# Kernel tuning notes

Hardware: AMD Instinct MI355X
Metric: run time of the kernel (lower is better)

Reference implementation:

```python
import jax, jax.numpy as jnp
import numpy as np

B, C, H, W = 2, 512, 64, 64
NH = 8
EPS = 1e-5


def setup_inputs() -> dict:
    key = jax.random.key(0)
    ks = jax.random.split(key, 4)
    s_in = 1.0 / np.sqrt(C)
    x = jax.random.normal(ks[0], (B, C, H, W), dtype=jnp.float32)
    qkv_w = jax.random.normal(ks[1], (3 * C, C), dtype=jnp.float32) * s_in
    qkv_b = jnp.zeros((3 * C,), dtype=jnp.float32)
    out_w = jax.random.normal(ks[2], (C, C), dtype=jnp.float32) * s_in
    out_b = jnp.zeros((C,), dtype=jnp.float32)
    ln_g = jnp.ones((C,), dtype=jnp.float32)
    ln_b = jnp.zeros((C,), dtype=jnp.float32)
    return {"x": x, "qkv_w": qkv_w, "qkv_b": qkv_b, "out_w": out_w,
            "out_b": out_b, "ln_g": ln_g, "ln_b": ln_b, "num_heads": NH}


def reference(x, qkv_w, qkv_b, out_w, out_b, ln_g, ln_b, num_heads):
    b, c, h, w = x.shape
    n = h * w
    hd = c // num_heads
    scale = hd ** -0.5

    # flatten spatial: [B, N, C]
    tokens = x.reshape(b, c, n).transpose(0, 2, 1)

    # fused QKV projection
    qkv = tokens @ qkv_w.T + qkv_b            # [B, N, 3C]
    q, k, v = jnp.split(qkv, 3, axis=-1)

    def heads(t):  # [B, N, C] -> [B, H, N, D]
        return t.reshape(b, n, num_heads, hd).transpose(0, 2, 1, 3)

    q, k, v = heads(q), heads(k), heads(v)

    # naive full attention (materializes [B, H, N, N] as in the original)
    scores = jnp.einsum('bhqd,bhkd->bhqk', q, k) * scale
    attn = jax.nn.softmax(scores, axis=-1)
    out = jnp.einsum('bhqk,bhkd->bhqd', attn, v)  # [B, H, N, D]

    out = out.transpose(0, 2, 1, 3).reshape(b, n, c)
    attended = out @ out_w.T + out_b          # [B, N, C]

    # residual + LayerNorm over channels
    res = attended + tokens
    mean = jnp.mean(res, axis=-1, keepdims=True)
    var = jnp.var(res, axis=-1, keepdims=True)
    y = (res - mean) * jax.lax.rsqrt(var + EPS) * ln_g + ln_b

    return y.transpose(0, 2, 1).reshape(b, c, h, w)
```

## Files before the change

### kernel.cpp

```cpp
#include <hip/hip_runtime.h>

#define BATCH 2
#define CH    512
#define NTOK  4096
#define NH    8
#define HD    64
#define MTOT  (BATCH*NTOK)

typedef __attribute__((ext_vector_type(8))) __bf16 bf16x8;
typedef __attribute__((ext_vector_type(4))) float  f32x4;
typedef __attribute__((ext_vector_type(4))) unsigned short u16x4;

static __device__ __forceinline__ f32x4 mfma16(bf16x8 a, bf16x8 b, f32x4 c) {
  return __builtin_amdgcn_mfma_f32_16x16x32_bf16(a, b, c, 0, 0, 0);
}

static __device__ __forceinline__ unsigned short f2bf(float f) {
  unsigned int u = __float_as_uint(f);
  u += 0x7fffu + ((u >> 16) & 1u);
  return (unsigned short)(u >> 16);
}

static __device__ __forceinline__ void gload_lds16(const unsigned short* g, unsigned short* l) {
  __builtin_amdgcn_global_load_lds((const __attribute__((address_space(1))) void*)g,
                                   (__attribute__((address_space(3))) void*)l, 16, 0, 0);
}

#define QSC 0.18033688011112042f

__global__ __launch_bounds__(256) void k_transpose(const float* __restrict__ x,
                                                   unsigned short* __restrict__ tokB) {
  __shared__ float tile[32][33];
  int b  = blockIdx.z;
  int n0 = blockIdx.x * 32;
  int c0 = blockIdx.y * 32;
  int tx = threadIdx.x & 31, ty = threadIdx.x >> 5;
#pragma unroll
  for (int i = 0; i < 4; i++) {
    int c = c0 + ty + 8 * i;
    tile[ty + 8 * i][tx] = x[((size_t)b * CH + c) * NTOK + n0 + tx];
  }
  __syncthreads();
#pragma unroll
  for (int i = 0; i < 4; i++) {
    int n = n0 + ty + 8 * i;
    int c = c0 + tx;
    tokB[((size_t)b * NTOK + n) * CH + c] = f2bf(tile[tx][ty + 8 * i]);
  }
}

__global__ __launch_bounds__(256) void k_castw(const float* __restrict__ w1,
                                               const float* __restrict__ w2,
                                               unsigned short* __restrict__ o1,
                                               unsigned short* __restrict__ o2) {
  int i = blockIdx.x * 256 + threadIdx.x;
  if (i < 3 * CH * CH) o1[i] = f2bf(w1[i]);
  else o2[i - 3 * CH * CH] = f2bf(w2[i - 3 * CH * CH]);
}

#define BK 64

static __device__ __forceinline__ void stage_g(const unsigned short* __restrict__ src,
                                               size_t row0, int k0,
                                               unsigned short* __restrict__ lds,
                                               int wid, int lane) {
  int sub = lane >> 3;
  int ch  = (lane & 7) ^ sub;
#pragma unroll
  for (int i = 0; i < 4; i++) {
    int rbase = 32 * wid + 8 * i;
    gload_lds16(&src[(row0 + rbase + sub) * 512 + k0 + ch * 8], &lds[rbase * BK]);
  }
}

static __device__ __forceinline__ void stage_g64(const unsigned short* __restrict__ src,
                                                 size_t row0, int k0,
                                                 unsigned short* __restrict__ lds,
                                                 int wid, int lane) {
  int sub = lane >> 3;
  int ch  = (lane & 7) ^ sub;
#pragma unroll
  for (int i = 0; i < 2; i++) {
    int rbase = 16 * wid + 8 * i;
    gload_lds16(&src[(row0 + rbase + sub) * 512 + k0 + ch * 8], &lds[rbase * BK]);
  }
}

static __device__ __forceinline__ bf16x8 frag_ld(const unsigned short* __restrict__ lds,
                                                 int row, int ks, int lane) {
  int ch = ((ks << 2) + (lane >> 4)) ^ (row & 7);
  return *reinterpret_cast<const bf16x8*>(&lds[row * BK + ch * 8]);
}

__global__ __launch_bounds__(256) void k_gemm_qkv(const unsigned short* __restrict__ A,
                                                  const unsigned short* __restrict__ W,
                                                  const float* __restrict__ bias,
                                                  unsigned short* __restrict__ qb,
                                                  unsigned short* __restrict__ kb,
                                                  unsigned short* __restrict__ vt) {
  __shared__ unsigned short lsA[128 * BK];
  __shared__ unsigned short lsB[128 * BK];
  int bm0 = blockIdx.x * 128;
  int bn0 = blockIdx.y * 128;
  int tid = threadIdx.x, lane = tid & 63, wid = tid >> 6;
  int wm = wid >> 1, wn = wid & 1;

  f32x4 acc[4][4];
  f32x4 zz = {0.f, 0.f, 0.f, 0.f};
#pragma unroll
  for (int i = 0; i < 4; i++)
#pragma unroll
    for (int j = 0; j < 4; j++) acc[i][j] = zz;

  for (int k0 = 0; k0 < 512; k0 += BK) {
    stage_g(A, (size_t)bm0, k0, lsA, wid, lane);
    stage_g(W, (size_t)bn0, k0, lsB, wid, lane);
    __syncthreads();
#pragma unroll
    for (int ks = 0; ks < 2; ks++) {
      bf16x8 af[4], bfr[4];
#pragma unroll
      for (int t = 0; t < 4; t++) {
        af[t]  = frag_ld(lsA, wm * 64 + t * 16 + (lane & 15), ks, lane);
        bfr[t] = frag_ld(lsB, wn * 64 + t * 16 + (lane & 15), ks, lane);
      }
#pragma unroll
      for (int mt = 0; mt < 4; mt++)
#pragma unroll
        for (int nt = 0; nt < 4; nt++) acc[mt][nt] = mfma16(af[mt], bfr[nt], acc[mt][nt]);
    }
    __syncthreads();
  }
#pragma unroll
  for (int nt = 0; nt < 4; nt++) {
    int j = bn0 + wn * 64 + nt * 16 + (lane & 15);
    float bj = bias[j];
    int which = j >> 9;
    int cp = j & 511;
    int h = cp >> 6, d = cp & 63;
    if (which == 2) {
#pragma unroll
      for (int mt = 0; mt < 4; mt++) {
        int m = bm0 + wm * 64 + mt * 16 + 4 * (lane >> 4);
        int b = m >> 12, n = m & 4095;
        u16x4 pk;
#pragma unroll
        for (int r = 0; r < 4; r++) pk[r] = f2bf(acc[mt][nt][r] + bj);
        *reinterpret_cast<u16x4*>(&vt[((size_t)((b * NH + h) * HD + d)) * NTOK + n]) = pk;
      }
    } else {
      unsigned short* dst = (which == 0) ? qb : kb;
      float sc = (which == 0) ? QSC : 1.0f;
#pragma unroll
      for (int mt = 0; mt < 4; mt++) {
#pragma unroll
        for (int r = 0; r < 4; r++) {
          int m = bm0 + wm * 64 + mt * 16 + 4 * (lane >> 4) + r;
          int b = m >> 12, n = m & 4095;
          dst[(((size_t)(b * NH + h) * NTOK + n) << 6) + d] = f2bf((acc[mt][nt][r] + bj) * sc);
        }
      }
    }
  }
}

#define KVB 128
#define NT  (NTOK / KVB)

static __device__ __forceinline__ void stage_kv(const unsigned short* __restrict__ Kp,
                                                const unsigned short* __restrict__ Vp,
                                                unsigned short* __restrict__ lk,
                                                unsigned short* __restrict__ lv,
                                                int kv0, int wid, int lane) {
  int sub = lane >> 3;
  int c7  = lane & 7;
  int sub4 = lane >> 4;
  int c15  = lane & 15;
#pragma unroll
  for (int i = 0; i < 4; i++) {
    int rbase = 32 * wid + 8 * i;
    int fk = (sub & 3) | ((i & 1) << 2);
    gload_lds16(&Kp[((size_t)(kv0 + rbase + sub) << 6) + ((c7 ^ fk) << 3)], &lk[rbase << 6]);
    int rbv = 16 * wid + 4 * i;
    int fv = 4 * i + sub4;
    gload_lds16(&Vp[(size_t)(rbv + sub4) * NTOK + kv0 + ((c15 ^ fv) << 3)], &lv[rbv << 7]);
  }
}

static __device__ __forceinline__ void attn_tile(const unsigned short* __restrict__ lk,
                                                 const unsigned short* __restrict__ lv,
                                                 int h,
                                                 const bf16x8 qf[2][2],
                                                 f32x4* oacc0, f32x4* oacc1,
                                                 f32x4& lacc0, f32x4& lacc1,
                                                 bf16x8 onesf, int g, int lr) {
  f32x4 zz = {0.f, 0.f, 0.f, 0.f};
  int l7 = lr & 7;
  int tbase = 8 * (lr >> 2) + (lr & 3);
  int kc0 = ((g ^ l7) << 3);
  int kc1 = (((4 + g) ^ l7) << 3);
  bf16x8 kf[4][2];
#pragma unroll
  for (int ct = 0; ct < 4; ct++) {
    int t = tbase + 4 * (ct >> 1) + 32 * (ct & 1);
    kf[ct][0] = *reinterpret_cast<const bf16x8*>(&lk[(t << 6) + kc0]);
    kf[ct][1] = *reinterpret_cast<const bf16x8*>(&lk[(t << 6) + kc1]);
  }
  f32x4 s0[4], s1[4];
#pragma unroll
  for (int ct = 0; ct < 4; ct++) {
    s0[ct] = zz; s1[ct] = zz;
#pragma unroll
    for (int ks = 0; ks < 2; ks++) {
      s0[ct] = mfma16(kf[ct][ks], qf[0][ks], s0[ct]);
      s1[ct] = mfma16(kf[ct][ks], qf[1][ks], s1[ct]);
    }
  }
  bf16x8 vf[4][2];
#pragma unroll
  for (int dt = 0; dt < 4; dt++) {
    int rowb = (dt * 16 + lr) << 7;
    vf[dt][0] = *reinterpret_cast<const bf16x8*>(&lv[rowb + ((((h << 3) + g) ^ lr) << 3)]);
    vf[dt][1] = *reinterpret_cast<const bf16x8*>(&lv[rowb + ((((h << 3) + 4 + g) ^ lr) << 3)]);
  }
#pragma unroll
  for (int ct = 0; ct < 4; ct++) {
#pragma unroll
    for (int r = 0; r < 4; r++) {
      s0[ct][r] = __builtin_exp2f(s0[ct][r]);
      s1[ct][r] = __builtin_exp2f(s1[ct][r]);
    }
  }
  unsigned int w0[4][2], w1[4][2];
#pragma unroll
  for (int ct = 0; ct < 4; ct++) {
    asm("v_cvt_pk_bf16_f32 %0, %1, %2" : "=v"(w0[ct][0]) : "v"(s0[ct][0]), "v"(s0[ct][1]));
    asm("v_cvt_pk_bf16_f32 %0, %1, %2" : "=v"(w0[ct][1]) : "v"(s0[ct][2]), "v"(s0[ct][3]));
    asm("v_cvt_pk_bf16_f32 %0, %1, %2" : "=v"(w1[ct][0]) : "v"(s1[ct][0]), "v"(s1[ct][1]));
    asm("v_cvt_pk_bf16_f32 %0, %1, %2" : "=v"(w1[ct][1]) : "v"(s1[ct][2]), "v"(s1[ct][3]));
  }
  union U { unsigned int w[4]; bf16x8 v; };
  U a0, a1, b0, b1;
  a0.w[0] = w0[0][0]; a0.w[1] = w0[0][1]; a0.w[2] = w0[2][0]; a0.w[3] = w0[2][1];
  a1.w[0] = w0[1][0]; a1.w[1] = w0[1][1]; a1.w[2] = w0[3][0]; a1.w[3] = w0[3][1];
  b0.w[0] = w1[0][0]; b0.w[1] = w1[0][1]; b0.w[2] = w1[2][0]; b0.w[3] = w1[2][1];
  b1.w[0] = w1[1][0]; b1.w[1] = w1[1][1]; b1.w[2] = w1[3][0]; b1.w[3] = w1[3][1];
#pragma unroll
  for (int dt = 0; dt < 4; dt++) {
    oacc0[dt] = mfma16(a0.v, vf[dt][0], oacc0[dt]);
    oacc0[dt] = mfma16(a1.v, vf[dt][1], oacc0[dt]);
    oacc1[dt] = mfma16(b0.v, vf[dt][0], oacc1[dt]);
    oacc1[dt] = mfma16(b1.v, vf[dt][1], oacc1[dt]);
  }
  lacc0 = mfma16(a0.v, onesf, lacc0);
  lacc0 = mfma16(a1.v, onesf, lacc0);
  lacc1 = mfma16(b0.v, onesf, lacc1);
  lacc1 = mfma16(b1.v, onesf, lacc1);
}

__global__ __launch_bounds__(256, 2) void k_attn(const unsigned short* __restrict__ Q,
                                                 const unsigned short* __restrict__ K,
                                                 const unsigned short* __restrict__ Vt,
                                                 unsigned short* __restrict__ O) {
  __shared__ unsigned short lsK[2][KVB * 64];
  __shared__ unsigned short lsV[2][64 * KVB];
  int gid = blockIdx.y * 32 + blockIdx.x;
  int vv  = (gid & 7) * 64 + (gid >> 3);
  int bh  = vv >> 5;
  int tid = threadIdx.x, lane = tid & 63, wid = tid >> 6;
  int g = lane >> 4, lr = lane & 15;
  int qw = (vv & 31) * 128 + wid * 32;
  const unsigned short* Qp = Q + (size_t)bh * NTOK * HD;
  const unsigned short* Kp = K + (size_t)bh * NTOK * HD;
  const unsigned short* Vp = Vt + (size_t)bh * HD * NTOK;
  unsigned short* K0 = &lsK[0][0]; unsigned short* K1 = &lsK[1][0];
  unsigned short* V0 = &lsV[0][0]; unsigned short* V1 = &lsV[1][0];

  union { unsigned short u[8]; bf16x8 v; } ou;
#pragma unroll
  for (int i = 0; i < 8; i++) ou.u[i] = 0x3F80;
  bf16x8 onesf = ou.v;

  bf16x8 qf[2][2];
#pragma unroll
  for (int sq = 0; sq < 2; sq++)
#pragma unroll
    for (int ks = 0; ks < 2; ks++)
      qf[sq][ks] = *reinterpret_cast<const bf16x8*>(
          &Qp[(size_t)(qw + sq * 16 + lr) * HD + ks * 32 + 8 * g]);

  f32x4 zz = {0.f, 0.f, 0.f, 0.f};
  f32x4 oacc0[4] = {zz, zz, zz, zz};
  f32x4 oacc1[4] = {zz, zz, zz, zz};
  f32x4 lacc0 = zz, lacc1 = zz;

  stage_kv(Kp, Vp, K0, V0, 0, wid, lane);
  __syncthreads();

  for (int t = 0; t < NT; t += 2) {
    stage_kv(Kp, Vp, K1, V1, (t + 1) * KVB, wid, lane);
    attn_tile(K0,        V0, 0, qf, oacc0, oacc1, lacc0, lacc1, onesf, g, lr);
    attn_tile(K0 + 4096, V0, 1, qf, oacc0, oacc1, lacc0, lacc1, onesf, g, lr);
    __syncthreads();
    if (t + 2 < NT) stage_kv(Kp, Vp, K0, V0, (t + 2) * KVB, wid, lane);
    attn_tile(K1,        V1, 0, qf, oacc0, oacc1, lacc0, lacc1, onesf, g, lr);
    attn_tile(K1 + 4096, V1, 1, qf, oacc0, oacc1, lacc0, lacc1, onesf, g, lr);
    __syncthreads();
  }
  int b2 = bh >> 3, h = bh & 7;
#pragma unroll
  for (int sq = 0; sq < 2; sq++) {
    f32x4* oacc = sq ? oacc1 : oacc0;
    f32x4  lacc = sq ? lacc1 : lacc0;
#pragma unroll
    for (int r = 0; r < 4; r++) {
      float inv = 1.0f / lacc[r];
      int n = qw + sq * 16 + 4 * g + r;
#pragma unroll
      for (int dt = 0; dt < 4; dt++) {
        int d = dt * 16 + lr;
        O[((size_t)(b2 * NTOK + n)) * CH + h * HD + d] = f2bf(oacc[dt][r] * inv);
      }
    }
  }
}

__global__ __launch_bounds__(256) void k_gemm_out(const unsigned short* __restrict__ A,
                                                  const unsigned short* __restrict__ W,
                                                  const float* __restrict__ bias,
                                                  const unsigned short* __restrict__ tokB,
                                                  unsigned short* __restrict__ res) {
  __shared__ unsigned short lsA[64 * BK];
  __shared__ unsigned short lsB[128 * BK];
  int bm0 = blockIdx.x * 64;
  int bn0 = blockIdx.y * 128;
  int tid = threadIdx.x, lane = tid & 63, wid = tid >> 6;
  int wm = wid >> 1, wn = wid & 1;

  f32x4 acc[2][4];
  f32x4 zz = {0.f, 0.f, 0.f, 0.f};
#pragma unroll
  for (int i = 0; i < 2; i++)
#pragma unroll
    for (int j = 0; j < 4; j++) acc[i][j] = zz;

  for (int k0 = 0; k0 < 512; k0 += BK) {
    stage_g64(A, (size_t)bm0, k0, lsA, wid, lane);
    stage_g(W, (size_t)bn0, k0, lsB, wid, lane);
    __syncthreads();
#pragma unroll
    for (int ks = 0; ks < 2; ks++) {
      bf16x8 af[2], bfr[4];
#pragma unroll
      for (int t = 0; t < 2; t++)
        af[t] = frag_ld(lsA, wm * 32 + t * 16 + (lane & 15), ks, lane);
#pragma unroll
      for (int t = 0; t < 4; t++)
        bfr[t] = frag_ld(lsB, wn * 64 + t * 16 + (lane & 15), ks, lane);
#pragma unroll
      for (int mt = 0; mt < 2; mt++)
#pragma unroll
        for (int nt = 0; nt < 4; nt++) acc[mt][nt] = mfma16(af[mt], bfr[nt], acc[mt][nt]);
    }
    __syncthreads();
  }
#pragma unroll
  for (int nt = 0; nt < 4; nt++) {
    int j = bn0 + wn * 64 + nt * 16 + (lane & 15);
    float bj = bias[j];
#pragma unroll
    for (int mt = 0; mt < 2; mt++) {
#pragma unroll
      for (int r = 0; r < 4; r++) {
        int m = bm0 + wm * 32 + mt * 16 + 4 * (lane >> 4) + r;
        size_t idx = (size_t)m * CH + j;
        float tk = __uint_as_float((unsigned int)tokB[idx] << 16);
        res[idx] = f2bf(acc[mt][nt][r] + bj + tk);
      }
    }
  }
}

__global__ __launch_bounds__(256) void k_ln(const unsigned short* __restrict__ res,
                                            const float* __restrict__ g,
                                            const float* __restrict__ bb,
                                            float* __restrict__ y) {
  __shared__ float smean[64], srstd[64];
  int m0 = blockIdx.x * 64;
  int tid = threadIdx.x, lane = tid & 63, wid = tid >> 6;
  for (int t = 0; t < 16; t++) {
    int idx = wid * 16 + t;
    uint4 v = *reinterpret_cast<const uint4*>(&res[(size_t)(m0 + idx) * CH + lane * 8]);
    unsigned int wv[4] = {v.x, v.y, v.z, v.w};
    float s = 0.f, ss = 0.f;
#pragma unroll
    for (int j = 0; j < 4; j++) {
      float lo = __uint_as_float(wv[j] << 16);
      float hi = __uint_as_float(wv[j] & 0xFFFF0000u);
      s += lo + hi; ss += lo * lo + hi * hi;
    }
#pragma unroll
    for (int off = 1; off < 64; off <<= 1) {
      s += __shfl_xor(s, off);
      ss += __shfl_xor(ss, off);
    }
    if (lane == 0) {
      float mean = s * (1.0f / CH);
      float var = ss * (1.0f / CH) - mean * mean;
      smean[idx] = mean;
      srstd[idx] = rsqrtf(var + 1e-5f);
    }
  }
  __syncthreads();
  int b = m0 >> 12, n0 = m0 & 4095;
  int tn = tid & 63;
  int cq = tid >> 6;
  float mn = smean[tn], rs = srstd[tn];
  const unsigned short* rrow = res + (size_t)(m0 + tn) * CH;
  float* yb = y + ((size_t)b * CH) * NTOK + n0 + tn;
#pragma unroll
  for (int i = 0; i < 16; i++) {
    int c = cq * 128 + i * 8;
    uint4 v = *reinterpret_cast<const uint4*>(&rrow[c]);
    unsigned int wv[4] = {v.x, v.y, v.z, v.w};
    float4 ga = *reinterpret_cast<const float4*>(&g[c]);
    float4 gb = *reinterpret_cast<const float4*>(&g[c + 4]);
    float4 ba = *reinterpret_cast<const float4*>(&bb[c]);
    float4 b4 = *reinterpret_cast<const float4*>(&bb[c + 4]);
    float gg[8] = {ga.x, ga.y, ga.z, ga.w, gb.x, gb.y, gb.z, gb.w};
    float bv[8] = {ba.x, ba.y, ba.z, ba.w, b4.x, b4.y, b4.z, b4.w};
#pragma unroll
    for (int j = 0; j < 4; j++) {
      float lo = __uint_as_float(wv[j] << 16);
      float hi = __uint_as_float(wv[j] & 0xFFFF0000u);
      yb[(size_t)(c + 2 * j) * NTOK]     = (lo - mn) * rs * gg[2 * j]     + bv[2 * j];
      yb[(size_t)(c + 2 * j + 1) * NTOK] = (hi - mn) * rs * gg[2 * j + 1] + bv[2 * j + 1];
    }
  }
}

extern "C" void kernel_launch(void* const* d_in, const int* in_sizes, int n_in,
                              void* d_out, int out_size, void* d_ws, size_t ws_size,
                              hipStream_t stream) {
  const float* x    = (const float*)d_in[0];
  const float* qkvw = (const float*)d_in[1];
  const float* qkvb = (const float*)d_in[2];
  const float* outw = (const float*)d_in[3];
  const float* outb = (const float*)d_in[4];
  const float* lng  = (const float*)d_in[5];
  const float* lnb  = (const float*)d_in[6];
  float* y = (float*)d_out;

  const size_t NC = (size_t)MTOT * CH;
  char* ws = (char*)d_ws;
  size_t off = 0;
  auto nxt = [&](size_t bytes) -> void* {
    void* p = ws + off;
    off += (bytes + 255) & ~(size_t)255;
    return p;
  };
  unsigned short* tokB = (unsigned short*)nxt(NC * 2);
  unsigned short* wqkv = (unsigned short*)nxt((size_t)3 * CH * CH * 2);
  unsigned short* wout = (unsigned short*)nxt((size_t)CH * CH * 2);
  unsigned short* qb   = (unsigned short*)nxt(NC * 2);
  unsigned short* kb   = (unsigned short*)nxt(NC * 2);
  unsigned short* vt   = (unsigned short*)nxt(NC * 2);
  unsigned short* ao   = (unsigned short*)nxt(NC * 2);
  unsigned short* resb = (unsigned short*)nxt(NC * 2);
  if (off > ws_size) return;

  k_transpose<<<dim3(NTOK / 32, CH / 32, BATCH), 256, 0, stream>>>(x, tokB);
  k_castw<<<(4 * CH * CH) / 256, 256, 0, stream>>>(qkvw, outw, wqkv, wout);
  k_gemm_qkv<<<dim3(MTOT / 128, (3 * CH) / 128), 256, 0, stream>>>(tokB, wqkv, qkvb, qb, kb, vt);
  k_attn<<<dim3(32, 16), 256, 0, stream>>>(qb, kb, vt, ao);
  k_gemm_out<<<dim3(MTOT / 64, CH / 128), 256, 0, stream>>>(ao, wout, outb, tokB, resb);
  k_ln<<<MTOT / 64, 256, 0, stream>>>(resb, lng, lnb, y);
}
```

Baseline: 164.0 us.

## Shrink attention tiles to 16 queries per wave and 64-key KV blocks

Restructures the attention kernel so each wave handles 16 query rows instead of 32, and each block stages 64 keys per step instead of 128. The V LDS layout and swizzle are simplified to match. The grid doubles to 1024 blocks, and launch bounds now target 4 blocks per CU, to raise occupancy and reduce register pressure. In exchange, K/V reuse per loaded tile is halved, so LDS reads and global traffic grow relative to MFMA work.

```diff
diff --git a/kernel.cpp b/kernel.cpp
--- a/kernel.cpp
+++ b/kernel.cpp
@@ -164,7 +164,7 @@
   }
 }
 
-#define KVB 128
+#define KVB 64
 #define NT  (NTOK / KVB)
 
 static __device__ __forceinline__ void stage_kv(const unsigned short* __restrict__ Kp,
@@ -174,25 +174,20 @@
                                                 int kv0, int wid, int lane) {
   int sub = lane >> 3;
   int c7  = lane & 7;
-  int sub4 = lane >> 4;
-  int c15  = lane & 15;
-#pragma unroll
-  for (int i = 0; i < 4; i++) {
-    int rbase = 32 * wid + 8 * i;
-    int fk = (sub & 3) | ((i & 1) << 2);
-    gload_lds16(&Kp[((size_t)(kv0 + rbase + sub) << 6) + ((c7 ^ fk) << 3)], &lk[rbase << 6]);
-    int rbv = 16 * wid + 4 * i;
-    int fv = 4 * i + sub4;
-    gload_lds16(&Vp[(size_t)(rbv + sub4) * NTOK + kv0 + ((c15 ^ fv) << 3)], &lv[rbv << 7]);
+#pragma unroll
+  for (int i = 0; i < 2; i++) {
+    int rbase = 16 * wid + 8 * i;
+    int row = rbase + sub;
+    int fk = (sub & 3) | (i << 2);
+    gload_lds16(&Kp[((size_t)(kv0 + row) << 6) + ((c7 ^ fk) << 3)], &lk[rbase << 6]);
+    gload_lds16(&Vp[(size_t)row * NTOK + kv0 + ((c7 ^ sub) << 3)], &lv[rbase << 6]);
   }
 }
 
 static __device__ __forceinline__ void attn_tile(const unsigned short* __restrict__ lk,
                                                  const unsigned short* __restrict__ lv,
-                                                 int h,
-                                                 const bf16x8 qf[2][2],
-                                                 f32x4* oacc0, f32x4* oacc1,
-                                                 f32x4& lacc0, f32x4& lacc1,
+                                                 const bf16x8 qf[2],
+                                                 f32x4* oacc, f32x4& lacc,
                                                  bf16x8 onesf, int g, int lr) {
   f32x4 zz = {0.f, 0.f, 0.f, 0.f};
   int l7 = lr & 7;
@@ -206,70 +201,55 @@
     kf[ct][0] = *reinterpret_cast<const bf16x8*>(&lk[(t << 6) + kc0]);
     kf[ct][1] = *reinterpret_cast<const bf16x8*>(&lk[(t << 6) + kc1]);
   }
-  f32x4 s0[4], s1[4];
+  f32x4 s[4];
 #pragma unroll
   for (int ct = 0; ct < 4; ct++) {
-    s0[ct] = zz; s1[ct] = zz;
-#pragma unroll
-    for (int ks = 0; ks < 2; ks++) {
-      s0[ct] = mfma16(kf[ct][ks], qf[0][ks], s0[ct]);
-      s1[ct] = mfma16(kf[ct][ks], qf[1][ks], s1[ct]);
-    }
+    s[ct] = mfma16(kf[ct][0], qf[0], zz);
+    s[ct] = mfma16(kf[ct][1], qf[1], s[ct]);
   }
   bf16x8 vf[4][2];
 #pragma unroll
   for (int dt = 0; dt < 4; dt++) {
-    int rowb = (dt * 16 + lr) << 7;
-    vf[dt][0] = *reinterpret_cast<const bf16x8*>(&lv[rowb + ((((h << 3) + g) ^ lr) << 3)]);
-    vf[dt][1] = *reinterpret_cast<const bf16x8*>(&lv[rowb + ((((h << 3) + 4 + g) ^ lr) << 3)]);
+    int rowb = (dt * 16 + lr) << 6;
+    vf[dt][0] = *reinterpret_cast<const bf16x8*>(&lv[rowb + kc0]);
+    vf[dt][1] = *reinterpret_cast<const bf16x8*>(&lv[rowb + kc1]);
   }
 #pragma unroll
   for (int ct = 0; ct < 4; ct++) {
 #pragma unroll
-    for (int r = 0; r < 4; r++) {
-      s0[ct][r] = __builtin_exp2f(s0[ct][r]);
-      s1[ct][r] = __builtin_exp2f(s1[ct][r]);
-    }
-  }
-  unsigned int w0[4][2], w1[4][2];
+    for (int r = 0; r < 4; r++) s[ct][r] = __builtin_exp2f(s[ct][r]);
+  }
+  unsigned int w[4][2];
 #pragma unroll
   for (int ct = 0; ct < 4; ct++) {
-    asm("v_cvt_pk_bf16_f32 %0, %1, %2" : "=v"(w0[ct][0]) : "v"(s0[ct][0]), "v"(s0[ct][1]));
-    asm("v_cvt_pk_bf16_f32 %0, %1, %2" : "=v"(w0[ct][1]) : "v"(s0[ct][2]), "v"(s0[ct][3]));
-    asm("v_cvt_pk_bf16_f32 %0, %1, %2" : "=v"(w1[ct][0]) : "v"(s1[ct][0]), "v"(s1[ct][1]));
-    asm("v_cvt_pk_bf16_f32 %0, %1, %2" : "=v"(w1[ct][1]) : "v"(s1[ct][2]), "v"(s1[ct][3]));
+    asm("v_cvt_pk_bf16_f32 %0, %1, %2" : "=v"(w[ct][0]) : "v"(s[ct][0]), "v"(s[ct][1]));
+    asm("v_cvt_pk_bf16_f32 %0, %1, %2" : "=v"(w[ct][1]) : "v"(s[ct][2]), "v"(s[ct][3]));
   }
   union U { unsigned int w[4]; bf16x8 v; };
-  U a0, a1, b0, b1;
-  a0.w[0] = w0[0][0]; a0.w[1] = w0[0][1]; a0.w[2] = w0[2][0]; a0.w[3] = w0[2][1];
-  a1.w[0] = w0[1][0]; a1.w[1] = w0[1][1]; a1.w[2] = w0[3][0]; a1.w[3] = w0[3][1];
-  b0.w[0] = w1[0][0]; b0.w[1] = w1[0][1]; b0.w[2] = w1[2][0]; b0.w[3] = w1[2][1];
-  b1.w[0] = w1[1][0]; b1.w[1] = w1[1][1]; b1.w[2] = w1[3][0]; b1.w[3] = w1[3][1];
+  U a0, a1;
+  a0.w[0] = w[0][0]; a0.w[1] = w[0][1]; a0.w[2] = w[2][0]; a0.w[3] = w[2][1];
+  a1.w[0] = w[1][0]; a1.w[1] = w[1][1]; a1.w[2] = w[3][0]; a1.w[3] = w[3][1];
 #pragma unroll
   for (int dt = 0; dt < 4; dt++) {
-    oacc0[dt] = mfma16(a0.v, vf[dt][0], oacc0[dt]);
-    oacc0[dt] = mfma16(a1.v, vf[dt][1], oacc0[dt]);
-    oacc1[dt] = mfma16(b0.v, vf[dt][0], oacc1[dt]);
-    oacc1[dt] = mfma16(b1.v, vf[dt][1], oacc1[dt]);
-  }
-  lacc0 = mfma16(a0.v, onesf, lacc0);
-  lacc0 = mfma16(a1.v, onesf, lacc0);
-  lacc1 = mfma16(b0.v, onesf, lacc1);
-  lacc1 = mfma16(b1.v, onesf, lacc1);
-}
-
-__global__ __launch_bounds__(256, 2) void k_attn(const unsigned short* __restrict__ Q,
+    oacc[dt] = mfma16(a0.v, vf[dt][0], oacc[dt]);
+    oacc[dt] = mfma16(a1.v, vf[dt][1], oacc[dt]);
+  }
+  lacc = mfma16(a0.v, onesf, lacc);
+  lacc = mfma16(a1.v, onesf, lacc);
+}
+
+__global__ __launch_bounds__(256, 4) void k_attn(const unsigned short* __restrict__ Q,
                                                  const unsigned short* __restrict__ K,
                                                  const unsigned short* __restrict__ Vt,
                                                  unsigned short* __restrict__ O) {
   __shared__ unsigned short lsK[2][KVB * 64];
   __shared__ unsigned short lsV[2][64 * KVB];
-  int gid = blockIdx.y * 32 + blockIdx.x;
-  int vv  = (gid & 7) * 64 + (gid >> 3);
-  int bh  = vv >> 5;
+  int gid = blockIdx.x;
+  int vv  = (gid & 7) * 128 + (gid >> 3);
+  int bh  = vv >> 6;
   int tid = threadIdx.x, lane = tid & 63, wid = tid >> 6;
   int g = lane >> 4, lr = lane & 15;
-  int qw = (vv & 31) * 128 + wid * 32;
+  int qw = (vv & 63) * 64 + wid * 16;
   const unsigned short* Qp = Q + (size_t)bh * NTOK * HD;
   const unsigned short* Kp = K + (size_t)bh * NTOK * HD;
   const unsigned short* Vp = Vt + (size_t)bh * HD * NTOK;
@@ -281,46 +261,36 @@
   for (int i = 0; i < 8; i++) ou.u[i] = 0x3F80;
   bf16x8 onesf = ou.v;
 
-  bf16x8 qf[2][2];
-#pragma unroll
-  for (int sq = 0; sq < 2; sq++)
-#pragma unroll
-    for (int ks = 0; ks < 2; ks++)
-      qf[sq][ks] = *reinterpret_cast<const bf16x8*>(
-          &Qp[(size_t)(qw + sq * 16 + lr) * HD + ks * 32 + 8 * g]);
+  bf16x8 qf[2];
+#pragma unroll
+  for (int ks = 0; ks < 2; ks++)
+    qf[ks] = *reinterpret_cast<const bf16x8*>(
+        &Qp[(size_t)(qw + lr) * HD + ks * 32 + 8 * g]);
 
   f32x4 zz = {0.f, 0.f, 0.f, 0.f};
-  f32x4 oacc0[4] = {zz, zz, zz, zz};
-  f32x4 oacc1[4] = {zz, zz, zz, zz};
-  f32x4 lacc0 = zz, lacc1 = zz;
+  f32x4 oacc[4] = {zz, zz, zz, zz};
+  f32x4 lacc = zz;
 
   stage_kv(Kp, Vp, K0, V0, 0, wid, lane);
   __syncthreads();
 
   for (int t = 0; t < NT; t += 2) {
     stage_kv(Kp, Vp, K1, V1, (t + 1) * KVB, wid, lane);
-    attn_tile(K0,        V0, 0, qf, oacc0, oacc1, lacc0, lacc1, onesf, g, lr);
-    attn_tile(K0 + 4096, V0, 1, qf, oacc0, oacc1, lacc0, lacc1, onesf, g, lr);
+    attn_tile(K0, V0, qf, oacc, lacc, onesf, g, lr);
     __syncthreads();
     if (t + 2 < NT) stage_kv(Kp, Vp, K0, V0, (t + 2) * KVB, wid, lane);
-    attn_tile(K1,        V1, 0, qf, oacc0, oacc1, lacc0, lacc1, onesf, g, lr);
-    attn_tile(K1 + 4096, V1, 1, qf, oacc0, oacc1, lacc0, lacc1, onesf, g, lr);
+    attn_tile(K1, V1, qf, oacc, lacc, onesf, g, lr);
     __syncthreads();
   }
   int b2 = bh >> 3, h = bh & 7;
 #pragma unroll
-  for (int sq = 0; sq < 2; sq++) {
-    f32x4* oacc = sq ? oacc1 : oacc0;
-    f32x4  lacc = sq ? lacc1 : lacc0;
-#pragma unroll
-    for (int r = 0; r < 4; r++) {
-      float inv = 1.0f / lacc[r];
-      int n = qw + sq * 16 + 4 * g + r;
-#pragma unroll
-      for (int dt = 0; dt < 4; dt++) {
-        int d = dt * 16 + lr;
-        O[((size_t)(b2 * NTOK + n)) * CH + h * HD + d] = f2bf(oacc[dt][r] * inv);
-      }
+  for (int r = 0; r < 4; r++) {
+    float inv = 1.0f / lacc[r];
+    int n = qw + 4 * g + r;
+#pragma unroll
+    for (int dt = 0; dt < 4; dt++) {
+      int d = dt * 16 + lr;
+      O[((size_t)(b2 * NTOK + n)) * CH + h * HD + d] = f2bf(oacc[dt][r] * inv);
     }
   }
 }
@@ -472,7 +442,7 @@
   k_transpose<<<dim3(NTOK / 32, CH / 32, BATCH), 256, 0, stream>>>(x, tokB);
   k_castw<<<(4 * CH * CH) / 256, 256, 0, stream>>>(qkvw, outw, wqkv, wout);
   k_gemm_qkv<<<dim3(MTOT / 128, (3 * CH) / 128), 256, 0, stream>>>(tokB, wqkv, qkvb, qb, kb, vt);
-  k_attn<<<dim3(32, 16), 256, 0, stream>>>(qb, kb, vt, ao);
+  k_attn<<<1024, 256, 0, stream>>>(qb, kb, vt, ao);
   k_gemm_out<<<dim3(MTOT / 64, CH / 128), 256, 0, stream>>>(ao, wout, outb, tokB, resb);
   k_ln<<<MTOT / 64, 256, 0, stream>>>(resb, lng, lnb, y);
 }
```

New measurement: 169.5 us. +3.3%, slower.

## Split KV tiles across wave pairs in attention and merge partial sums via LDS

Applied to the files above, without the earlier changes.

The attention kernel now gives each block 64 queries instead of 128 and launches 1024 blocks. Within a block, pairs of waves split each 64-key tile in half, and the two halves' partial output and denominator sums are combined through LDS at the end. The KV tile shrinks to 64, which cuts LDS use and permits four blocks per CU, aiming for more parallelism and occupancy. In exchange, each K/V tile is reused by fewer queries, so global traffic and the number of syncs per key rise, and there is an extra reduction step.

```diff
diff --git a/kernel.cpp b/kernel.cpp
--- a/kernel.cpp
+++ b/kernel.cpp
@@ -164,7 +164,7 @@
   }
 }
 
-#define KVB 128
+#define KVB 64
 #define NT  (NTOK / KVB)
 
 static __device__ __forceinline__ void stage_kv(const unsigned short* __restrict__ Kp,
@@ -174,102 +174,90 @@
                                                 int kv0, int wid, int lane) {
   int sub = lane >> 3;
   int c7  = lane & 7;
-  int sub4 = lane >> 4;
-  int c15  = lane & 15;
-#pragma unroll
-  for (int i = 0; i < 4; i++) {
-    int rbase = 32 * wid + 8 * i;
-    int fk = (sub & 3) | ((i & 1) << 2);
-    gload_lds16(&Kp[((size_t)(kv0 + rbase + sub) << 6) + ((c7 ^ fk) << 3)], &lk[rbase << 6]);
-    int rbv = 16 * wid + 4 * i;
-    int fv = 4 * i + sub4;
-    gload_lds16(&Vp[(size_t)(rbv + sub4) * NTOK + kv0 + ((c15 ^ fv) << 3)], &lv[rbv << 7]);
+#pragma unroll
+  for (int i = 0; i < 2; i++) {
+    int rbase = 16 * wid + 8 * i;
+    int row = rbase + sub;
+    int fk = (sub & 3) | (i << 2);
+    gload_lds16(&Kp[((size_t)(kv0 + row) << 6) + ((c7 ^ fk) << 3)], &lk[rbase << 6]);
+    gload_lds16(&Vp[(size_t)row * NTOK + kv0 + ((c7 ^ sub) << 3)], &lv[rbase << 6]);
   }
 }
 
 static __device__ __forceinline__ void attn_tile(const unsigned short* __restrict__ lk,
                                                  const unsigned short* __restrict__ lv,
-                                                 int h,
+                                                 int half,
                                                  const bf16x8 qf[2][2],
                                                  f32x4* oacc0, f32x4* oacc1,
                                                  f32x4& lacc0, f32x4& lacc1,
                                                  bf16x8 onesf, int g, int lr) {
   f32x4 zz = {0.f, 0.f, 0.f, 0.f};
   int l7 = lr & 7;
-  int tbase = 8 * (lr >> 2) + (lr & 3);
-  int kc0 = ((g ^ l7) << 3);
-  int kc1 = (((4 + g) ^ l7) << 3);
-  bf16x8 kf[4][2];
-#pragma unroll
-  for (int ct = 0; ct < 4; ct++) {
-    int t = tbase + 4 * (ct >> 1) + 32 * (ct & 1);
+  int tbase = 32 * half + 8 * (lr >> 2) + (lr & 3);
+  int kc0 = (g ^ l7) << 3;
+  int kc1 = ((4 + g) ^ l7) << 3;
+  bf16x8 kf[2][2];
+#pragma unroll
+  for (int ct = 0; ct < 2; ct++) {
+    int t = tbase + 4 * ct;
     kf[ct][0] = *reinterpret_cast<const bf16x8*>(&lk[(t << 6) + kc0]);
     kf[ct][1] = *reinterpret_cast<const bf16x8*>(&lk[(t << 6) + kc1]);
   }
-  f32x4 s0[4], s1[4];
-#pragma unroll
-  for (int ct = 0; ct < 4; ct++) {
-    s0[ct] = zz; s1[ct] = zz;
-#pragma unroll
-    for (int ks = 0; ks < 2; ks++) {
-      s0[ct] = mfma16(kf[ct][ks], qf[0][ks], s0[ct]);
-      s1[ct] = mfma16(kf[ct][ks], qf[1][ks], s1[ct]);
-    }
-  }
-  bf16x8 vf[4][2];
-#pragma unroll
-  for (int dt = 0; dt < 4; dt++) {
-    int rowb = (dt * 16 + lr) << 7;
-    vf[dt][0] = *reinterpret_cast<const bf16x8*>(&lv[rowb + ((((h << 3) + g) ^ lr) << 3)]);
-    vf[dt][1] = *reinterpret_cast<const bf16x8*>(&lv[rowb + ((((h << 3) + 4 + g) ^ lr) << 3)]);
-  }
-#pragma unroll
-  for (int ct = 0; ct < 4; ct++) {
+  f32x4 s0[2], s1[2];
+#pragma unroll
+  for (int ct = 0; ct < 2; ct++) {
+    s0[ct] = mfma16(kf[ct][0], qf[0][0], zz);
+    s0[ct] = mfma16(kf[ct][1], qf[0][1], s0[ct]);
+    s1[ct] = mfma16(kf[ct][0], qf[1][0], zz);
+    s1[ct] = mfma16(kf[ct][1], qf[1][1], s1[ct]);
+  }
+  bf16x8 vf[4];
+  int vc = (((half << 2) + g) ^ l7) << 3;
+#pragma unroll
+  for (int dt = 0; dt < 4; dt++)
+    vf[dt] = *reinterpret_cast<const bf16x8*>(&lv[((dt * 16 + lr) << 6) + vc]);
+#pragma unroll
+  for (int ct = 0; ct < 2; ct++) {
 #pragma unroll
     for (int r = 0; r < 4; r++) {
       s0[ct][r] = __builtin_exp2f(s0[ct][r]);
       s1[ct][r] = __builtin_exp2f(s1[ct][r]);
     }
   }
-  unsigned int w0[4][2], w1[4][2];
-#pragma unroll
-  for (int ct = 0; ct < 4; ct++) {
+  unsigned int w0[2][2], w1[2][2];
+#pragma unroll
+  for (int ct = 0; ct < 2; ct++) {
     asm("v_cvt_pk_bf16_f32 %0, %1, %2" : "=v"(w0[ct][0]) : "v"(s0[ct][0]), "v"(s0[ct][1]));
     asm("v_cvt_pk_bf16_f32 %0, %1, %2" : "=v"(w0[ct][1]) : "v"(s0[ct][2]), "v"(s0[ct][3]));
     asm("v_cvt_pk_bf16_f32 %0, %1, %2" : "=v"(w1[ct][0]) : "v"(s1[ct][0]), "v"(s1[ct][1]));
     asm("v_cvt_pk_bf16_f32 %0, %1, %2" : "=v"(w1[ct][1]) : "v"(s1[ct][2]), "v"(s1[ct][3]));
   }
   union U { unsigned int w[4]; bf16x8 v; };
-  U a0, a1, b0, b1;
-  a0.w[0] = w0[0][0]; a0.w[1] = w0[0][1]; a0.w[2] = w0[2][0]; a0.w[3] = w0[2][1];
-  a1.w[0] = w0[1][0]; a1.w[1] = w0[1][1]; a1.w[2] = w0[3][0]; a1.w[3] = w0[3][1];
-  b0.w[0] = w1[0][0]; b0.w[1] = w1[0][1]; b0.w[2] = w1[2][0]; b0.w[3] = w1[2][1];
-  b1.w[0] = w1[1][0]; b1.w[1] = w1[1][1]; b1.w[2] = w1[3][0]; b1.w[3] = w1[3][1];
+  U a0, b0;
+  a0.w[0] = w0[0][0]; a0.w[1] = w0[0][1]; a0.w[2] = w0[1][0]; a0.w[3] = w0[1][1];
+  b0.w[0] = w1[0][0]; b0.w[1] = w1[0][1]; b0.w[2] = w1[1][0]; b0.w[3] = w1[1][1];
 #pragma unroll
   for (int dt = 0; dt < 4; dt++) {
-    oacc0[dt] = mfma16(a0.v, vf[dt][0], oacc0[dt]);
-    oacc0[dt] = mfma16(a1.v, vf[dt][1], oacc0[dt]);
-    oacc1[dt] = mfma16(b0.v, vf[dt][0], oacc1[dt]);
-    oacc1[dt] = mfma16(b1.v, vf[dt][1], oacc1[dt]);
+    oacc0[dt] = mfma16(a0.v, vf[dt], oacc0[dt]);
+    oacc1[dt] = mfma16(b0.v, vf[dt], oacc1[dt]);
   }
   lacc0 = mfma16(a0.v, onesf, lacc0);
-  lacc0 = mfma16(a1.v, onesf, lacc0);
   lacc1 = mfma16(b0.v, onesf, lacc1);
-  lacc1 = mfma16(b1.v, onesf, lacc1);
-}
-
-__global__ __launch_bounds__(256, 2) void k_attn(const unsigned short* __restrict__ Q,
+}
+
+__global__ __launch_bounds__(256, 4) void k_attn(const unsigned short* __restrict__ Q,
                                                  const unsigned short* __restrict__ K,
                                                  const unsigned short* __restrict__ Vt,
                                                  unsigned short* __restrict__ O) {
   __shared__ unsigned short lsK[2][KVB * 64];
   __shared__ unsigned short lsV[2][64 * KVB];
-  int gid = blockIdx.y * 32 + blockIdx.x;
-  int vv  = (gid & 7) * 64 + (gid >> 3);
-  int bh  = vv >> 5;
+  int gid = blockIdx.x;
+  int vv  = (gid & 7) * 128 + (gid >> 3);
+  int bh  = vv >> 6;
   int tid = threadIdx.x, lane = tid & 63, wid = tid >> 6;
+  int pair = wid >> 1, half = wid & 1;
   int g = lane >> 4, lr = lane & 15;
-  int qw = (vv & 31) * 128 + wid * 32;
+  int qw = (vv & 63) * 64 + pair * 32;
   const unsigned short* Qp = Q + (size_t)bh * NTOK * HD;
   const unsigned short* Kp = K + (size_t)bh * NTOK * HD;
   const unsigned short* Vp = Vt + (size_t)bh * HD * NTOK;
@@ -299,27 +287,46 @@
 
   for (int t = 0; t < NT; t += 2) {
     stage_kv(Kp, Vp, K1, V1, (t + 1) * KVB, wid, lane);
-    attn_tile(K0,        V0, 0, qf, oacc0, oacc1, lacc0, lacc1, onesf, g, lr);
-    attn_tile(K0 + 4096, V0, 1, qf, oacc0, oacc1, lacc0, lacc1, onesf, g, lr);
+    attn_tile(K0, V0, half, qf, oacc0, oacc1, lacc0, lacc1, onesf, g, lr);
     __syncthreads();
     if (t + 2 < NT) stage_kv(Kp, Vp, K0, V0, (t + 2) * KVB, wid, lane);
-    attn_tile(K1,        V1, 0, qf, oacc0, oacc1, lacc0, lacc1, onesf, g, lr);
-    attn_tile(K1 + 4096, V1, 1, qf, oacc0, oacc1, lacc0, lacc1, onesf, g, lr);
-    __syncthreads();
-  }
-  int b2 = bh >> 3, h = bh & 7;
-#pragma unroll
-  for (int sq = 0; sq < 2; sq++) {
-    f32x4* oacc = sq ? oacc1 : oacc0;
-    f32x4  lacc = sq ? lacc1 : lacc0;
-#pragma unroll
-    for (int r = 0; r < 4; r++) {
-      float inv = 1.0f / lacc[r];
-      int n = qw + sq * 16 + 4 * g + r;
-#pragma unroll
-      for (int dt = 0; dt < 4; dt++) {
-        int d = dt * 16 + lr;
-        O[((size_t)(b2 * NTOK + n)) * CH + h * HD + d] = f2bf(oacc[dt][r] * inv);
+    attn_tile(K1, V1, half, qf, oacc0, oacc1, lacc0, lacc1, onesf, g, lr);
+    __syncthreads();
+  }
+  float* mO = (float*)&lsK[0][0];
+  float* mL = (float*)&lsV[0][0];
+  if (half) {
+#pragma unroll
+    for (int sq = 0; sq < 2; sq++) {
+      f32x4* oacc = sq ? oacc1 : oacc0;
+      f32x4  lacc = sq ? lacc1 : lacc0;
+#pragma unroll
+      for (int r = 0; r < 4; r++) {
+        int q = pair * 32 + sq * 16 + 4 * g + r;
+#pragma unroll
+        for (int dt = 0; dt < 4; dt++) mO[(q << 6) + dt * 16 + lr] = oacc[dt][r];
+        if (lr == 0) mL[q] = lacc[r];
+      }
+    }
+  }
+  __syncthreads();
+  if (!half) {
+    int b2 = bh >> 3, h = bh & 7;
+#pragma unroll
+    for (int sq = 0; sq < 2; sq++) {
+      f32x4* oacc = sq ? oacc1 : oacc0;
+      f32x4  lacc = sq ? lacc1 : lacc0;
+#pragma unroll
+      for (int r = 0; r < 4; r++) {
+        int q = pair * 32 + sq * 16 + 4 * g + r;
+        float inv = 1.0f / (lacc[r] + mL[q]);
+        int n = qw + sq * 16 + 4 * g + r;
+#pragma unroll
+        for (int dt = 0; dt < 4; dt++) {
+          int d = dt * 16 + lr;
+          float o = oacc[dt][r] + mO[(q << 6) + dt * 16 + lr];
+          O[((size_t)(b2 * NTOK + n)) * CH + h * HD + d] = f2bf(o * inv);
+        }
       }
     }
   }
@@ -472,7 +479,7 @@
   k_transpose<<<dim3(NTOK / 32, CH / 32, BATCH), 256, 0, stream>>>(x, tokB);
   k_castw<<<(4 * CH * CH) / 256, 256, 0, stream>>>(qkvw, outw, wqkv, wout);
   k_gemm_qkv<<<dim3(MTOT / 128, (3 * CH) / 128), 256, 0, stream>>>(tokB, wqkv, qkvb, qb, kb, vt);
-  k_attn<<<dim3(32, 16), 256, 0, stream>>>(qb, kb, vt, ao);
+  k_attn<<<1024, 256, 0, stream>>>(qb, kb, vt, ao);
   k_gemm_out<<<dim3(MTOT / 64, CH / 128), 256, 0, stream>>>(ao, wout, outb, tokB, resb);
   k_ln<<<MTOT / 64, 256, 0, stream>>>(resb, lng, lnb, y);
 }
```

After: 167.2 us. About the same (+1.9%).
